# Kernel optimization log

Measured on AMD Instinct MI355X. Metric: run time of the kernel, lower is better.

Reference implementation:

```python
import jax, jax.numpy as jnp
import numpy as np

B, T, IN_DIM, H = 128, 512, 128, 512


def _lstm_layer(x, W_ih, W_hh, b_ih, b_hh):
    """Single-layer batch-first LSTM (PyTorch gate order i,f,g,o).
    x: [B, T, D]. Returns (outputs [B, T, H], h_T [B, H], c_T [B, H])."""
    Bsz = x.shape[0]
    Hdim = W_hh.shape[1]
    # Precompute the input contribution for all timesteps: [T, B, 4H]
    xg = jnp.einsum('btd,gd->tbg', x, W_ih) + (b_ih + b_hh)

    def step(carry, xg_t):
        h, c = carry
        gates = xg_t + h @ W_hh.T  # [B, 4H]
        i, f, g, o = jnp.split(gates, 4, axis=-1)
        i = jax.nn.sigmoid(i)
        f = jax.nn.sigmoid(f)
        g = jnp.tanh(g)
        o = jax.nn.sigmoid(o)
        c = f * c + i * g
        h = o * jnp.tanh(c)
        return (h, c), h

    h0 = jnp.zeros((Bsz, Hdim), dtype=x.dtype)
    c0 = jnp.zeros((Bsz, Hdim), dtype=x.dtype)
    (hT, cT), outs = jax.lax.scan(step, (h0, c0), xg)
    return jnp.transpose(outs, (1, 0, 2)), hT, cT


def setup_inputs() -> dict:
    key = jax.random.key(0)
    ks = jax.random.split(key, 9)
    s1 = 1.0 / np.sqrt(H)
    inp = {
        'x': jax.random.normal(ks[0], (B, T, IN_DIM), dtype=jnp.float32),
        'W_ih1': jax.random.uniform(ks[1], (4 * H, IN_DIM), jnp.float32, -s1, s1),
        'W_hh1': jax.random.uniform(ks[2], (4 * H, H), jnp.float32, -s1, s1),
        'b_ih1': jax.random.uniform(ks[3], (4 * H,), jnp.float32, -s1, s1),
        'b_hh1': jax.random.uniform(ks[4], (4 * H,), jnp.float32, -s1, s1),
        'W_ih2': jax.random.uniform(ks[5], (4 * H, H), jnp.float32, -s1, s1),
        'W_hh2': jax.random.uniform(ks[6], (4 * H, H), jnp.float32, -s1, s1),
        'b_ih2': jax.random.uniform(ks[7], (4 * H,), jnp.float32, -s1, s1),
        'b_hh2': jax.random.uniform(ks[8], (4 * H,), jnp.float32, -s1, s1),
    }
    return inp


def reference(x, W_ih1, W_hh1, b_ih1, b_hh1, W_ih2, W_hh2, b_ih2, b_hh2):
    out1, _, _ = _lstm_layer(x, W_ih1, W_hh1, b_ih1, b_hh1)
    _, hT, cT = _lstm_layer(out1, W_ih2, W_hh2, b_ih2, b_hh2)
    # Match torch nn.LSTM final-state shape: [num_layers*dirs=1, B, H]
    return hT[None, :, :], cT[None, :, :]
```

## Files before the change

### kernel.cpp

```cpp
#include <hip/hip_runtime.h>
#include <stdint.h>
#include <stddef.h>


typedef __attribute__((ext_vector_type(8))) short short8;
typedef __attribute__((ext_vector_type(4))) float f32x4;

#define DEV static __device__ __forceinline__
#define SCOPE_AGENT __HIP_MEMORY_SCOPE_AGENT

constexpr int TSEQ = 512;
constexpr int DIN  = 128;
constexpr int HDIM = 512;
constexpr int NCL  = 8;
constexpr int BB   = 16;
constexpr int NJ   = 32;
constexpr int COLS = 16;

DEV unsigned short f2bf(float f) {
  unsigned u = __float_as_uint(f);
  u += 0x7fffu + ((u >> 16) & 1u);
  return (unsigned short)(u >> 16);
}
DEV short8 pack8(float4 a, float4 b) {
  short8 r;
  r[0] = (short)f2bf(a.x); r[1] = (short)f2bf(a.y);
  r[2] = (short)f2bf(a.z); r[3] = (short)f2bf(a.w);
  r[4] = (short)f2bf(b.x); r[5] = (short)f2bf(b.y);
  r[6] = (short)f2bf(b.z); r[7] = (short)f2bf(b.w);
  return r;
}
DEV f32x4 mfma16(short8 a, short8 b, f32x4 c) {
  return __builtin_amdgcn_mfma_f32_16x16x32_bf16(a, b, c, 0, 0, 0);
}
DEV float sigf(float v) { return 1.f / (1.f + __expf(-v)); }
DEV float tanh_(float v) {
  v = fminf(20.f, fmaxf(-20.f, v));
  float e = __expf(2.f * v);
  return (e - 1.f) / (e + 1.f);
}

__global__ void zero_ws(unsigned* p, int n) {
  int i = blockIdx.x * 256 + threadIdx.x;
  if (i < n)
    __hip_atomic_store(p + i, 0u, __ATOMIC_RELAXED, SCOPE_AGENT);
}

#define SWZ(row, idx) ((idx) ^ (((row) & 15) << 3))

__global__ __launch_bounds__(256, 1) void lstm_persist(
    const float* __restrict__ x,
    const float* __restrict__ Wih1, const float* __restrict__ Whh1,
    const float* __restrict__ bih1, const float* __restrict__ bhh1,
    const float* __restrict__ Wih2, const float* __restrict__ Whh2,
    const float* __restrict__ bih2, const float* __restrict__ bhh2,
    float* __restrict__ out,
    unsigned short* __restrict__ buf1,
    unsigned short* __restrict__ buf2,
    unsigned* __restrict__ flags)
{
  __shared__ short xs [16 * DIN];
  __shared__ short h1s[16 * HDIM];
  __shared__ short h2s[16 * HDIM];
  __shared__ float red1[4 * 16 * 66];
  __shared__ float red2[4 * 16 * 66];
  __shared__ float bias1s[64], bias2s[64];

  const int tid  = threadIdx.x;
  const int lane = tid & 63;
  const int lm   = lane & 15;
  const int lq   = lane >> 4;
  const int kq   = tid >> 6;

  const int bid     = blockIdx.x;
  const int cluster = bid & 7;
  const int j       = bid >> 3;
  const int cb      = cluster * BB;
  unsigned* cnt     = flags + cluster;

  short8 wf1[4][5];
  short8 wf2[4][8];
  #pragma unroll
  for (int g = 0; g < 4; ++g) {
    const int gr = g * HDIM + j * COLS + lm;
    #pragma unroll
    for (int sl = 0; sl < 5; ++sl) {
      const int k0 = (kq * 5 + sl) * 32 + 8 * lq;
      const float* src = (k0 < DIN) ? (Wih1 + (size_t)gr * DIN + k0)
                                    : (Whh1 + (size_t)gr * HDIM + (k0 - DIN));
      wf1[g][sl] = pack8(*(const float4*)src, *(const float4*)(src + 4));
    }
    #pragma unroll
    for (int sl = 0; sl < 8; ++sl) {
      const int k0 = (kq * 8 + sl) * 32 + 8 * lq;
      const float* src = (k0 < HDIM) ? (Wih2 + (size_t)gr * HDIM + k0)
                                     : (Whh2 + (size_t)gr * HDIM + (k0 - HDIM));
      wf2[g][sl] = pack8(*(const float4*)src, *(const float4*)(src + 4));
    }
  }
  if (tid < 64) {
    const int g = tid >> 4, nn = tid & 15;
    const int gr = g * HDIM + j * COLS + nn;
    bias1s[tid] = bih1[gr] + bhh1[gr];
    bias2s[tid] = bih2[gr] + bhh2[gr];
  }

  const int pm = tid >> 4, pnn = tid & 15;
  float c1 = 0.f, c2 = 0.f;

  for (int it = 0; it <= TSEQ; ++it) {
    if (it < TSEQ) {
      const int row = tid >> 4, kc = tid & 15;
      const float* xp = x + ((size_t)(cb + row) * TSEQ + it) * DIN + kc * 8;
      *(short8*)(&xs[SWZ(row, row * DIN + kc * 8)]) =
          pack8(*(const float4*)xp, *(const float4*)(xp + 4));
    }

    if (it > 0) {
      if (tid == 0) {
        const unsigned thr = (unsigned)(NJ * it);
        while (__hip_atomic_load(cnt, __ATOMIC_RELAXED, SCOPE_AGENT) < thr)
          __builtin_amdgcn_s_sleep(1);
      }
      __syncthreads();
    }

    const unsigned short* h1r =
        buf1 + (size_t)(((it + 1) & 1) * NCL + cluster) * BB * HDIM;
    const unsigned short* h2r =
        buf2 + (size_t)((it & 1) * NCL + cluster) * BB * HDIM;
    {
      unsigned long long t[8];
      #pragma unroll
      for (int ci = 0; ci < 4; ++ci) {
        const int c = ci * 256 + tid;
        const int row = c >> 6, kc = c & 63;
        const unsigned long long* s =
            (const unsigned long long*)(h1r + (size_t)row * HDIM + kc * 8);
        t[2 * ci]     = __hip_atomic_load(s,     __ATOMIC_RELAXED, SCOPE_AGENT);
        t[2 * ci + 1] = __hip_atomic_load(s + 1, __ATOMIC_RELAXED, SCOPE_AGENT);
      }
      #pragma unroll
      for (int ci = 0; ci < 4; ++ci) {
        const int c = ci * 256 + tid;
        const int row = c >> 6, kc = c & 63;
        unsigned long long* d =
            (unsigned long long*)&h1s[SWZ(row, row * HDIM + kc * 8)];
        d[0] = t[2 * ci]; d[1] = t[2 * ci + 1];
      }
      #pragma unroll
      for (int ci = 0; ci < 4; ++ci) {
        const int c = ci * 256 + tid;
        const int row = c >> 6, kc = c & 63;
        const unsigned long long* s =
            (const unsigned long long*)(h2r + (size_t)row * HDIM + kc * 8);
        t[2 * ci]     = __hip_atomic_load(s,     __ATOMIC_RELAXED, SCOPE_AGENT);
        t[2 * ci + 1] = __hip_atomic_load(s + 1, __ATOMIC_RELAXED, SCOPE_AGENT);
      }
      #pragma unroll
      for (int ci = 0; ci < 4; ++ci) {
        const int c = ci * 256 + tid;
        const int row = c >> 6, kc = c & 63;
        unsigned long long* d =
            (unsigned long long*)&h2s[SWZ(row, row * HDIM + kc * 8)];
        d[0] = t[2 * ci]; d[1] = t[2 * ci + 1];
      }
    }
    __syncthreads();

    f32x4 z = {0.f, 0.f, 0.f, 0.f};
    f32x4 acc1[4] = {z, z, z, z};
    f32x4 acc2[4] = {z, z, z, z};
    if (it < TSEQ) {
      #pragma unroll
      for (int sl = 0; sl < 5; ++sl) {
        const int s = kq * 5 + sl;
        short8 a;
        if (s < 4)
          a = *(const short8*)(&xs[SWZ(lm, lm * DIN + s * 32 + 8 * lq)]);
        else
          a = *(const short8*)(&h1s[SWZ(lm, lm * HDIM + (s - 4) * 32 + 8 * lq)]);
        #pragma unroll
        for (int g = 0; g < 4; ++g) acc1[g] = mfma16(a, wf1[g][sl], acc1[g]);
      }
    }
    if (it >= 1) {
      #pragma unroll
      for (int sl = 0; sl < 8; ++sl) {
        const int s2 = kq * 8 + sl;
        short8 a;
        if (s2 < 16)
          a = *(const short8*)(&h1s[SWZ(lm, lm * HDIM + s2 * 32 + 8 * lq)]);
        else
          a = *(const short8*)(&h2s[SWZ(lm, lm * HDIM + (s2 - 16) * 32 + 8 * lq)]);
        #pragma unroll
        for (int g = 0; g < 4; ++g) acc2[g] = mfma16(a, wf2[g][sl], acc2[g]);
      }
    }
    if (it < TSEQ) {
      #pragma unroll
      for (int g = 0; g < 4; ++g)
        #pragma unroll
        for (int r = 0; r < 4; ++r)
          red1[(kq * 16 + lq * 4 + r) * 66 + g * 16 + lm] = acc1[g][r];
    }
    if (it >= 1) {
      #pragma unroll
      for (int g = 0; g < 4; ++g)
        #pragma unroll
        for (int r = 0; r < 4; ++r)
          red2[(kq * 16 + lq * 4 + r) * 66 + g * 16 + lm] = acc2[g][r];
    }
    __syncthreads();

    if (it < TSEQ) {
      float p[4];
      #pragma unroll
      for (int g = 0; g < 4; ++g) {
        float v = bias1s[g * 16 + pnn];
        #pragma unroll
        for (int q = 0; q < 4; ++q) v += red1[(q * 16 + pm) * 66 + g * 16 + pnn];
        p[g] = v;
      }
      const float i_ = sigf(p[0]), f_ = sigf(p[1]);
      const float g_ = tanh_(p[2]), o_ = sigf(p[3]);
      c1 = f_ * c1 + i_ * g_;
      const float h1v = o_ * tanh_(c1);
      unsigned short* w = buf1 + (size_t)((it & 1) * NCL + cluster) * BB * HDIM;
      __hip_atomic_store(&w[pm * HDIM + j * COLS + pnn], f2bf(h1v),
                         __ATOMIC_RELAXED, SCOPE_AGENT);
    }
    if (it >= 1) {
      float p[4];
      #pragma unroll
      for (int g = 0; g < 4; ++g) {
        float v = bias2s[g * 16 + pnn];
        #pragma unroll
        for (int q = 0; q < 4; ++q) v += red2[(q * 16 + pm) * 66 + g * 16 + pnn];
        p[g] = v;
      }
      const float i_ = sigf(p[0]), f_ = sigf(p[1]);
      const float g_ = tanh_(p[2]), o_ = sigf(p[3]);
      c2 = f_ * c2 + i_ * g_;
      const float h2v = o_ * tanh_(c2);
      if (it < TSEQ) {
        unsigned short* w =
            buf2 + (size_t)(((it + 1) & 1) * NCL + cluster) * BB * HDIM;
        __hip_atomic_store(&w[pm * HDIM + j * COLS + pnn], f2bf(h2v),
                           __ATOMIC_RELAXED, SCOPE_AGENT);
      } else {
        const int b = cb + pm;
        out[(size_t)b * HDIM + j * COLS + pnn] = h2v;
        out[(size_t)128 * HDIM + (size_t)b * HDIM + j * COLS + pnn] = c2;
      }
    }
    __syncthreads();

    if (tid == 0 && it < TSEQ)
      __hip_atomic_fetch_add(cnt, 1u, __ATOMIC_RELAXED, SCOPE_AGENT);
  }
}

extern "C" void kernel_launch(void* const* d_in, const int* in_sizes, int n_in,
                              void* d_out, int out_size, void* d_ws, size_t ws_size,
                              hipStream_t stream) {
  const float* x    = (const float*)d_in[0];
  const float* Wih1 = (const float*)d_in[1];
  const float* Whh1 = (const float*)d_in[2];
  const float* bih1 = (const float*)d_in[3];
  const float* bhh1 = (const float*)d_in[4];
  const float* Wih2 = (const float*)d_in[5];
  const float* Whh2 = (const float*)d_in[6];
  const float* bih2 = (const float*)d_in[7];
  const float* bhh2 = (const float*)d_in[8];
  float* out = (float*)d_out;

  const size_t bufElems = (size_t)2 * NCL * BB * HDIM;
  unsigned short* buf1 = (unsigned short*)d_ws;
  unsigned short* buf2 = buf1 + bufElems;
  unsigned* flags = (unsigned*)(buf2 + bufElems);

  const int nzero = (int)((bufElems * 2 * 2 + NCL * 4) / 4);
  zero_ws<<<(nzero + 255) / 256, 256, 0, stream>>>((unsigned*)d_ws, nzero);
  lstm_persist<<<256, 256, 0, stream>>>(x, Wih1, Whh1, bih1, bhh1,
                                        Wih2, Whh2, bih2, bhh2,
                                        out, buf1, buf2, flags);
}
```

Baseline: 2.254 ms.

## Replace atomic counter barrier with per-block flags and split layer signals

Replaces the single fetch-add counter per cluster with per-block flag slots: each block stores its layer-1 flag right after writing h1, before the layer-2 epilogue, and its layer-2 flag at the end. One wavefront polls all 64 flags in parallel with a wave-wide vote instead of a single thread polling one counter. The intent is to cut atomic contention and let layer-1 progress be published earlier, so the critical path shrinks. It also adds an LDS padding array, presumably to guarantee one block per CU, at the cost of an extra barrier per step.

```diff
diff --git a/kernel.cpp b/kernel.cpp
--- a/kernel.cpp
+++ b/kernel.cpp
@@ -5,6 +5,7 @@
 
 typedef __attribute__((ext_vector_type(8))) short short8;
 typedef __attribute__((ext_vector_type(4))) float f32x4;
+typedef unsigned long long u64;
 
 #define DEV static __device__ __forceinline__
 #define SCOPE_AGENT __HIP_MEMORY_SCOPE_AGENT
@@ -29,6 +30,10 @@
   r[4] = (short)f2bf(b.x); r[5] = (short)f2bf(b.y);
   r[6] = (short)f2bf(b.z); r[7] = (short)f2bf(b.w);
   return r;
+}
+DEV short8 mk8(u64 lo, u64 hi) {
+  union { u64 q[2]; short8 v; } u;
+  u.q[0] = lo; u.q[1] = hi; return u.v;
 }
 DEV f32x4 mfma16(short8 a, short8 b, f32x4 c) {
   return __builtin_amdgcn_mfma_f32_16x16x32_bf16(a, b, c, 0, 0, 0);
@@ -65,6 +70,7 @@
   __shared__ float red1[4 * 16 * 66];
   __shared__ float red2[4 * 16 * 66];
   __shared__ float bias1s[64], bias2s[64];
+  __shared__ float occpad[3072];
 
   const int tid  = threadIdx.x;
   const int lane = tid & 63;
@@ -76,7 +82,8 @@
   const int cluster = bid & 7;
   const int j       = bid >> 3;
   const int cb      = cluster * BB;
-  unsigned* cnt     = flags + cluster;
+
+  asm volatile("" :: "v"(&occpad[tid & 1023]));
 
   short8 wf1[4][5];
   short8 wf2[4][8];
@@ -109,7 +116,10 @@
   float c1 = 0.f, c2 = 0.f;
 
   for (int it = 0; it <= TSEQ; ++it) {
-    if (it < TSEQ) {
+    const bool l1 = (it < TSEQ);
+    const bool l2 = (it >= 1);
+
+    if (l1) {
       const int row = tid >> 4, kc = tid & 15;
       const float* xp = x + ((size_t)(cb + row) * TSEQ + it) * DIN + kc * 8;
       *(short8*)(&xs[SWZ(row, row * DIN + kc * 8)]) =
@@ -117,10 +127,14 @@
     }
 
     if (it > 0) {
-      if (tid == 0) {
-        const unsigned thr = (unsigned)(NJ * it);
-        while (__hip_atomic_load(cnt, __ATOMIC_RELAXED, SCOPE_AGENT) < thr)
+      if (kq == 0) {
+        const unsigned* fl = flags + cluster * 64 + lane;
+        const unsigned tgt = (lane < NJ) ? (unsigned)it : (unsigned)(it - 1);
+        while (true) {
+          unsigned v = __hip_atomic_load(fl, __ATOMIC_RELAXED, SCOPE_AGENT);
+          if (__all((int)(v >= tgt))) break;
           __builtin_amdgcn_s_sleep(1);
+        }
       }
       __syncthreads();
     }
@@ -130,13 +144,12 @@
     const unsigned short* h2r =
         buf2 + (size_t)((it & 1) * NCL + cluster) * BB * HDIM;
     {
-      unsigned long long t[8];
+      u64 t[8];
       #pragma unroll
       for (int ci = 0; ci < 4; ++ci) {
         const int c = ci * 256 + tid;
         const int row = c >> 6, kc = c & 63;
-        const unsigned long long* s =
-            (const unsigned long long*)(h1r + (size_t)row * HDIM + kc * 8);
+        const u64* s = (const u64*)(h1r + (size_t)row * HDIM + kc * 8);
         t[2 * ci]     = __hip_atomic_load(s,     __ATOMIC_RELAXED, SCOPE_AGENT);
         t[2 * ci + 1] = __hip_atomic_load(s + 1, __ATOMIC_RELAXED, SCOPE_AGENT);
       }
@@ -144,16 +157,14 @@
       for (int ci = 0; ci < 4; ++ci) {
         const int c = ci * 256 + tid;
         const int row = c >> 6, kc = c & 63;
-        unsigned long long* d =
-            (unsigned long long*)&h1s[SWZ(row, row * HDIM + kc * 8)];
+        u64* d = (u64*)&h1s[SWZ(row, row * HDIM + kc * 8)];
         d[0] = t[2 * ci]; d[1] = t[2 * ci + 1];
       }
       #pragma unroll
       for (int ci = 0; ci < 4; ++ci) {
         const int c = ci * 256 + tid;
         const int row = c >> 6, kc = c & 63;
-        const unsigned long long* s =
-            (const unsigned long long*)(h2r + (size_t)row * HDIM + kc * 8);
+        const u64* s = (const u64*)(h2r + (size_t)row * HDIM + kc * 8);
         t[2 * ci]     = __hip_atomic_load(s,     __ATOMIC_RELAXED, SCOPE_AGENT);
         t[2 * ci + 1] = __hip_atomic_load(s + 1, __ATOMIC_RELAXED, SCOPE_AGENT);
       }
@@ -161,8 +172,7 @@
       for (int ci = 0; ci < 4; ++ci) {
         const int c = ci * 256 + tid;
         const int row = c >> 6, kc = c & 63;
-        unsigned long long* d =
-            (unsigned long long*)&h2s[SWZ(row, row * HDIM + kc * 8)];
+        u64* d = (u64*)&h2s[SWZ(row, row * HDIM + kc * 8)];
         d[0] = t[2 * ci]; d[1] = t[2 * ci + 1];
       }
     }
@@ -171,7 +181,7 @@
     f32x4 z = {0.f, 0.f, 0.f, 0.f};
     f32x4 acc1[4] = {z, z, z, z};
     f32x4 acc2[4] = {z, z, z, z};
-    if (it < TSEQ) {
+    if (l1) {
       #pragma unroll
       for (int sl = 0; sl < 5; ++sl) {
         const int s = kq * 5 + sl;
@@ -184,7 +194,7 @@
         for (int g = 0; g < 4; ++g) acc1[g] = mfma16(a, wf1[g][sl], acc1[g]);
       }
     }
-    if (it >= 1) {
+    if (l2) {
       #pragma unroll
       for (int sl = 0; sl < 8; ++sl) {
         const int s2 = kq * 8 + sl;
@@ -197,14 +207,14 @@
         for (int g = 0; g < 4; ++g) acc2[g] = mfma16(a, wf2[g][sl], acc2[g]);
       }
     }
-    if (it < TSEQ) {
+    if (l1) {
       #pragma unroll
       for (int g = 0; g < 4; ++g)
         #pragma unroll
         for (int r = 0; r < 4; ++r)
           red1[(kq * 16 + lq * 4 + r) * 66 + g * 16 + lm] = acc1[g][r];
     }
-    if (it >= 1) {
+    if (l2) {
       #pragma unroll
       for (int g = 0; g < 4; ++g)
         #pragma unroll
@@ -213,7 +223,7 @@
     }
     __syncthreads();
 
-    if (it < TSEQ) {
+    if (l1) {
       float p[4];
       #pragma unroll
       for (int g = 0; g < 4; ++g) {
@@ -226,11 +236,16 @@
       const float g_ = tanh_(p[2]), o_ = sigf(p[3]);
       c1 = f_ * c1 + i_ * g_;
       const float h1v = o_ * tanh_(c1);
-      unsigned short* w = buf1 + (size_t)((it & 1) * NCL + cluster) * BB * HDIM;
-      __hip_atomic_store(&w[pm * HDIM + j * COLS + pnn], f2bf(h1v),
+      unsigned short* wp = buf1 + (size_t)((it & 1) * NCL + cluster) * BB * HDIM;
+      __hip_atomic_store(&wp[pm * HDIM + j * COLS + pnn], f2bf(h1v),
                          __ATOMIC_RELAXED, SCOPE_AGENT);
     }
-    if (it >= 1) {
+    __syncthreads();
+    if (tid == 0 && l1)
+      __hip_atomic_store(flags + cluster * 64 + j, (unsigned)(it + 1),
+                         __ATOMIC_RELAXED, SCOPE_AGENT);
+
+    if (l2) {
       float p[4];
       #pragma unroll
       for (int g = 0; g < 4; ++g) {
@@ -243,10 +258,10 @@
       const float g_ = tanh_(p[2]), o_ = sigf(p[3]);
       c2 = f_ * c2 + i_ * g_;
       const float h2v = o_ * tanh_(c2);
-      if (it < TSEQ) {
-        unsigned short* w =
+      if (l1) {
+        unsigned short* wp =
             buf2 + (size_t)(((it + 1) & 1) * NCL + cluster) * BB * HDIM;
-        __hip_atomic_store(&w[pm * HDIM + j * COLS + pnn], f2bf(h2v),
+        __hip_atomic_store(&wp[pm * HDIM + j * COLS + pnn], f2bf(h2v),
                            __ATOMIC_RELAXED, SCOPE_AGENT);
       } else {
         const int b = cb + pm;
@@ -255,9 +270,9 @@
       }
     }
     __syncthreads();
-
-    if (tid == 0 && it < TSEQ)
-      __hip_atomic_fetch_add(cnt, 1u, __ATOMIC_RELAXED, SCOPE_AGENT);
+    if (tid == 0 && l1 && l2)
+      __hip_atomic_store(flags + cluster * 64 + NJ + j, (unsigned)it,
+                         __ATOMIC_RELAXED, SCOPE_AGENT);
   }
 }
 
@@ -280,7 +295,7 @@
   unsigned short* buf2 = buf1 + bufElems;
   unsigned* flags = (unsigned*)(buf2 + bufElems);
 
-  const int nzero = (int)((bufElems * 2 * 2 + NCL * 4) / 4);
+  const int nzero = (int)((bufElems * 2 * 2 + NCL * 64 * 4) / 4);
   zero_ws<<<(nzero + 255) / 256, 256, 0, stream>>>((unsigned*)d_ws, nzero);
   lstm_persist<<<256, 256, 0, stream>>>(x, Wih1, Whh1, bih1, bhh1,
                                         Wih2, Whh2, bih2, bhh2,
```

Result: faster. 1.986 ms (-11.9%).
